# Performance work log

Hardware: AMD Instinct MI355X
Metric: run time of the kernel (lower is better)

Reference implementation:

```python
import jax, jax.numpy as jnp
import numpy as np


def _bs_matrix(n):
    # Kronecker product of n copies of the 2x2 beam-splitter unitary.
    bs = (1.0 / np.sqrt(2.0)) * np.array([[1 + 0j, 0 + 1j], [0 + 1j, 1 + 0j]], dtype=np.complex128)
    M = np.array([[1.0 + 0j]], dtype=np.complex128)
    for _ in range(n):
        M = np.kron(M, bs)
    return jnp.asarray(M, dtype=jnp.complex64)  # [2^n, 2^n]


def _phase_shifts(phi0, phi1, n):
    # Equivalent to phase_shifts_to_tensor_product_space_v2:
    # phi[i] = sum_q (phi1[q] if bit_{n-1-q}(i) else phi0[q]); returns exp(i*phi).
    N = 2 ** n
    bits = (jnp.arange(N)[:, None] >> (n - 1 - jnp.arange(n))[None, :]) & 1  # [N, n]
    bits = bits.astype(phi0.dtype)
    phi = jnp.sum(bits * phi1 + (1.0 - bits) * phi0, axis=-1)  # [N]
    return jax.lax.complex(jnp.cos(phi), jnp.sin(phi))


def setup_inputs() -> dict:
    n = 12
    N = 2 ** n
    B = 2048
    key = jax.random.key(0)
    kx, ka, kb, kt, kp = jax.random.split(key, 5)
    TWO_PI = 2.0 * np.pi
    return {
        "x": jax.random.normal(kx, (B, 2, N), dtype=jnp.float32),
        "alphas": jax.random.uniform(ka, (n,), dtype=jnp.float32, minval=0.0, maxval=TWO_PI),
        "betas": jax.random.uniform(kb, (n,), dtype=jnp.float32, minval=0.0, maxval=TWO_PI),
        "thetas": jax.random.uniform(kt, (n,), dtype=jnp.float32, minval=0.0, maxval=TWO_PI),
        "phis": jax.random.uniform(kp, (n,), dtype=jnp.float32, minval=0.0, maxval=TWO_PI),
    }


def reference(x, alphas, betas, thetas, phis):
    n = alphas.shape[0]
    bs = _bs_matrix(n)  # [N, N] complex
    input_shifts = _phase_shifts(alphas, betas, n)                       # [N]
    theta_shifts = _phase_shifts(thetas, jnp.zeros_like(thetas), n)      # [N]
    phi_shifts = _phase_shifts(phis, jnp.zeros_like(phis), n)            # [N]

    z = jax.lax.complex(x[:, 0, :], x[:, 1, :])  # [B, N]
    out = (input_shifts * z) @ bs
    out = (theta_shifts * out) @ bs
    out = phi_shifts * out
    return jnp.stack([jnp.real(out), jnp.imag(out)], axis=1)  # [B, 2, N]
```

## Files before the change

### kernel.cpp

```cpp
#include <hip/hip_runtime.h>
#include <math.h>

#define NQ 12
#define NN 4096

typedef float f2 __attribute__((ext_vector_type(2)));

__device__ __forceinline__ float2 cmulh(float2 a, float2 b) {
    return make_float2(a.x * b.x - a.y * b.y, a.x * b.y + a.y * b.x);
}

__device__ __forceinline__ void cmac_pk(f2& acc, f2 m, f2 b) {
    asm("v_pk_fma_f32 %0, %1, %2, %0 op_sel:[0,0,0] op_sel_hi:[0,1,1]\n\t"
        "v_pk_fma_f32 %0, %1, %2, %0 op_sel:[1,1,0] op_sel_hi:[1,0,1] neg_lo:[1,0,0]"
        : "+v"(acc) : "s"(m), "v"(b));
}
__device__ __forceinline__ void cmul_pk(f2& r, f2 m, f2 b) {
    asm("v_pk_mul_f32 %0, %1, %2 op_sel:[0,0] op_sel_hi:[0,1]\n\t"
        "v_pk_fma_f32 %0, %1, %2, %0 op_sel:[1,1,0] op_sel_hi:[1,0,1] neg_lo:[1,0,0]"
        : "=&v"(r) : "s"(m), "v"(b));
}

template<int D>
__device__ __forceinline__ void stagepk8(f2 (&v)[8], f2 m00, f2 m01, f2 m10, f2 m11) {
    #pragma unroll
    for (int s = 0; s < 8; ++s) {
        if (s & D) continue;
        f2 va = v[s], vb = v[s | D];
        f2 r0, r1;
        cmul_pk(r0, m00, va); cmac_pk(r0, m01, vb);
        cmul_pk(r1, m10, va); cmac_pk(r1, m11, vb);
        v[s] = r0; v[s | D] = r1;
    }
}

__global__ void setup_mats(const float* __restrict__ alphas,
                           const float* __restrict__ betas,
                           const float* __restrict__ thetas,
                           const float* __restrict__ phis,
                           float2* __restrict__ Mg) {
    int t = threadIdx.x;
    if (t < NQ) {
        int p = t, q = NQ - 1 - p;
        float sa, ca, sb, cb, st, ct, sf, cf;
        sincosf(alphas[q], &sa, &ca);
        sincosf(betas[q],  &sb, &cb);
        sincosf(thetas[q], &st, &ct);
        sincosf(phis[q],   &sf, &cf);
        float2 A  = make_float2(ca, sa);
        float2 Bb = make_float2(cb, sb);
        float2 F  = make_float2(cf, sf);
        float2 Tm  = make_float2(0.5f * (ct - 1.0f), 0.5f * st);
        float2 Tp  = make_float2(0.5f * (ct + 1.0f), 0.5f * st);
        float2 iTp = make_float2(-Tp.y, Tp.x);
        Mg[p * 4 + 0] = cmulh(cmulh(F, Tm), A);
        Mg[p * 4 + 1] = cmulh(cmulh(F, iTp), Bb);
        Mg[p * 4 + 2] = cmulh(iTp, A);
        Mg[p * 4 + 3] = cmulh(make_float2(-Tm.x, -Tm.y), Bb);
    }
}

__global__ __launch_bounds__(512, 8) void sq_layer(const float* __restrict__ x,
                                                   const float2* __restrict__ Mgf,
                                                   float* __restrict__ out) {
    __shared__ f2 lds[4608];
    const int T = threadIdx.x;
    const f2* Mg = (const f2*)Mgf;
    const size_t row0 = (size_t)blockIdx.x * 2;

    const float* px = x + row0 * (2 * NN) + (T << 3);
    float4 ra = *reinterpret_cast<const float4*>(px);
    float4 rb = *reinterpret_cast<const float4*>(px + 4);
    float4 ia = *reinterpret_cast<const float4*>(px + NN);
    float4 ib = *reinterpret_cast<const float4*>(px + NN + 4);

    #pragma unroll
    for (int r = 0; r < 2; ++r) {
        f2 v[8];
        v[0] = f2{ra.x, ia.x}; v[1] = f2{ra.y, ia.y};
        v[2] = f2{ra.z, ia.z}; v[3] = f2{ra.w, ia.w};
        v[4] = f2{rb.x, ib.x}; v[5] = f2{rb.y, ib.y};
        v[6] = f2{rb.z, ib.z}; v[7] = f2{rb.w, ib.w};

        if (r == 0) {
            const float* pn = px + 2 * NN;
            ra = *reinterpret_cast<const float4*>(pn);
            rb = *reinterpret_cast<const float4*>(pn + 4);
            ia = *reinterpret_cast<const float4*>(pn + NN);
            ib = *reinterpret_cast<const float4*>(pn + NN + 4);
        }

        stagepk8<1>(v, Mg[0],  Mg[1],  Mg[2],  Mg[3]);
        stagepk8<2>(v, Mg[4],  Mg[5],  Mg[6],  Mg[7]);
        stagepk8<4>(v, Mg[8],  Mg[9],  Mg[10], Mg[11]);

        {
            f2* wp = lds + 9 * T;
            #pragma unroll
            for (int s = 0; s < 8; ++s) wp[s] = v[s];
        }
        {
            const f2* rp = lds + 72 * (T >> 3) + (T & 7);
            #pragma unroll
            for (int s = 0; s < 8; ++s) v[s] = rp[9 * s];
        }

        stagepk8<1>(v, Mg[12], Mg[13], Mg[14], Mg[15]);
        stagepk8<2>(v, Mg[16], Mg[17], Mg[18], Mg[19]);
        stagepk8<4>(v, Mg[20], Mg[21], Mg[22], Mg[23]);

        {
            f2* wp = lds + 72 * (T >> 3) + (T & 7);
            #pragma unroll
            for (int s = 0; s < 8; ++s) wp[9 * s] = v[s];
        }
        {
            const f2* rp = lds + 576 * (T >> 6) + (T & 63) + ((T & 63) >> 3);
            #pragma unroll
            for (int s = 0; s < 8; ++s) v[s] = rp[72 * s];
        }

        stagepk8<1>(v, Mg[24], Mg[25], Mg[26], Mg[27]);
        stagepk8<2>(v, Mg[28], Mg[29], Mg[30], Mg[31]);
        stagepk8<4>(v, Mg[32], Mg[33], Mg[34], Mg[35]);

        {
            f2* wp = lds + 576 * (T >> 6) + (T & 63) + ((T & 63) >> 3);
            #pragma unroll
            for (int s = 0; s < 8; ++s) wp[72 * s] = v[s];
        }
        __syncthreads();
        {
            const f2* rp = lds + T + (T >> 3);
            #pragma unroll
            for (int s = 0; s < 8; ++s) v[s] = rp[576 * s];
        }
        if (r == 0) __syncthreads();

        stagepk8<1>(v, Mg[36], Mg[37], Mg[38], Mg[39]);
        stagepk8<2>(v, Mg[40], Mg[41], Mg[42], Mg[43]);
        stagepk8<4>(v, Mg[44], Mg[45], Mg[46], Mg[47]);

        {
            float* po = out + (row0 + r) * (2 * NN);
            #pragma unroll
            for (int s = 0; s < 8; ++s) {
                int i = (s << 9) | T;
                __builtin_nontemporal_store(v[s].x, po + i);
                __builtin_nontemporal_store(v[s].y, po + NN + i);
            }
        }
    }
}

extern "C" void kernel_launch(void* const* d_in, const int* in_sizes, int n_in,
                              void* d_out, int out_size, void* d_ws, size_t ws_size,
                              hipStream_t stream) {
    const float* x      = (const float*)d_in[0];
    const float* alphas = (const float*)d_in[1];
    const float* betas  = (const float*)d_in[2];
    const float* thetas = (const float*)d_in[3];
    const float* phis   = (const float*)d_in[4];
    float* out = (float*)d_out;
    float2* Mg = (float2*)d_ws;

    const int B = in_sizes[0] / (2 * NN);

    hipLaunchKernelGGL(setup_mats, dim3(1), dim3(64), 0, stream,
                       alphas, betas, thetas, phis, Mg);
    hipLaunchKernelGGL(sq_layer, dim3(B / 2), dim3(512), 0, stream,
                       x, (const float2*)Mg, out);
}
```

Measured before the change: 31.53 us.

## Fuse per-qubit matrix setup into main kernel via shared memory

Drops the separate setup kernel launch: each block now computes the 12 per-qubit 2x2 gate matrices itself with sincos in 12 threads, stores them in shared memory, and synchronises before use. Both rows' input loads are issued up front so their latency overlaps the setup. The inline asm operands switch from scalar to vector registers because the matrices now come from LDS. This removes one launch and its dependency gap, but every block repeats the trig work, adds a barrier, and holds more registers for the early loads.

```diff
diff --git a/kernel.cpp b/kernel.cpp
--- a/kernel.cpp
+++ b/kernel.cpp
@@ -13,12 +13,12 @@
 __device__ __forceinline__ void cmac_pk(f2& acc, f2 m, f2 b) {
     asm("v_pk_fma_f32 %0, %1, %2, %0 op_sel:[0,0,0] op_sel_hi:[0,1,1]\n\t"
         "v_pk_fma_f32 %0, %1, %2, %0 op_sel:[1,1,0] op_sel_hi:[1,0,1] neg_lo:[1,0,0]"
-        : "+v"(acc) : "s"(m), "v"(b));
+        : "+v"(acc) : "v"(m), "v"(b));
 }
 __device__ __forceinline__ void cmul_pk(f2& r, f2 m, f2 b) {
     asm("v_pk_mul_f32 %0, %1, %2 op_sel:[0,0] op_sel_hi:[0,1]\n\t"
         "v_pk_fma_f32 %0, %1, %2, %0 op_sel:[1,1,0] op_sel_hi:[1,0,1] neg_lo:[1,0,0]"
-        : "=&v"(r) : "s"(m), "v"(b));
+        : "=&v"(r) : "v"(m), "v"(b));
 }
 
 template<int D>
@@ -34,14 +34,29 @@
     }
 }
 
-__global__ void setup_mats(const float* __restrict__ alphas,
-                           const float* __restrict__ betas,
-                           const float* __restrict__ thetas,
-                           const float* __restrict__ phis,
-                           float2* __restrict__ Mg) {
-    int t = threadIdx.x;
-    if (t < NQ) {
-        int p = t, q = NQ - 1 - p;
+__global__ __launch_bounds__(512, 8) void sq_layer(const float* __restrict__ x,
+                                                   float* __restrict__ out,
+                                                   const float* __restrict__ alphas,
+                                                   const float* __restrict__ betas,
+                                                   const float* __restrict__ thetas,
+                                                   const float* __restrict__ phis) {
+    __shared__ f2 lds[4608];
+    __shared__ f2 Msh[48];
+    const int T = threadIdx.x;
+    const size_t row0 = (size_t)blockIdx.x * 2;
+
+    const float* px = x + row0 * (2 * NN) + (T << 3);
+    float4 ra0 = *reinterpret_cast<const float4*>(px);
+    float4 rb0 = *reinterpret_cast<const float4*>(px + 4);
+    float4 ia0 = *reinterpret_cast<const float4*>(px + NN);
+    float4 ib0 = *reinterpret_cast<const float4*>(px + NN + 4);
+    float4 ra1 = *reinterpret_cast<const float4*>(px + 2 * NN);
+    float4 rb1 = *reinterpret_cast<const float4*>(px + 2 * NN + 4);
+    float4 ia1 = *reinterpret_cast<const float4*>(px + 3 * NN);
+    float4 ib1 = *reinterpret_cast<const float4*>(px + 3 * NN + 4);
+
+    if (T < NQ) {
+        int p = T, q = NQ - 1 - p;
         float sa, ca, sb, cb, st, ct, sf, cf;
         sincosf(alphas[q], &sa, &ca);
         sincosf(betas[q],  &sb, &cb);
@@ -53,46 +68,32 @@
         float2 Tm  = make_float2(0.5f * (ct - 1.0f), 0.5f * st);
         float2 Tp  = make_float2(0.5f * (ct + 1.0f), 0.5f * st);
         float2 iTp = make_float2(-Tp.y, Tp.x);
-        Mg[p * 4 + 0] = cmulh(cmulh(F, Tm), A);
-        Mg[p * 4 + 1] = cmulh(cmulh(F, iTp), Bb);
-        Mg[p * 4 + 2] = cmulh(iTp, A);
-        Mg[p * 4 + 3] = cmulh(make_float2(-Tm.x, -Tm.y), Bb);
+        float2 m00 = cmulh(cmulh(F, Tm), A);
+        float2 m01 = cmulh(cmulh(F, iTp), Bb);
+        float2 m10 = cmulh(iTp, A);
+        float2 m11 = cmulh(make_float2(-Tm.x, -Tm.y), Bb);
+        Msh[p * 4 + 0] = f2{m00.x, m00.y};
+        Msh[p * 4 + 1] = f2{m01.x, m01.y};
+        Msh[p * 4 + 2] = f2{m10.x, m10.y};
+        Msh[p * 4 + 3] = f2{m11.x, m11.y};
     }
-}
-
-__global__ __launch_bounds__(512, 8) void sq_layer(const float* __restrict__ x,
-                                                   const float2* __restrict__ Mgf,
-                                                   float* __restrict__ out) {
-    __shared__ f2 lds[4608];
-    const int T = threadIdx.x;
-    const f2* Mg = (const f2*)Mgf;
-    const size_t row0 = (size_t)blockIdx.x * 2;
-
-    const float* px = x + row0 * (2 * NN) + (T << 3);
-    float4 ra = *reinterpret_cast<const float4*>(px);
-    float4 rb = *reinterpret_cast<const float4*>(px + 4);
-    float4 ia = *reinterpret_cast<const float4*>(px + NN);
-    float4 ib = *reinterpret_cast<const float4*>(px + NN + 4);
+    __syncthreads();
 
     #pragma unroll
     for (int r = 0; r < 2; ++r) {
         f2 v[8];
+        float4 ra = (r == 0) ? ra0 : ra1;
+        float4 rb = (r == 0) ? rb0 : rb1;
+        float4 ia = (r == 0) ? ia0 : ia1;
+        float4 ib = (r == 0) ? ib0 : ib1;
         v[0] = f2{ra.x, ia.x}; v[1] = f2{ra.y, ia.y};
         v[2] = f2{ra.z, ia.z}; v[3] = f2{ra.w, ia.w};
         v[4] = f2{rb.x, ib.x}; v[5] = f2{rb.y, ib.y};
         v[6] = f2{rb.z, ib.z}; v[7] = f2{rb.w, ib.w};
 
-        if (r == 0) {
-            const float* pn = px + 2 * NN;
-            ra = *reinterpret_cast<const float4*>(pn);
-            rb = *reinterpret_cast<const float4*>(pn + 4);
-            ia = *reinterpret_cast<const float4*>(pn + NN);
-            ib = *reinterpret_cast<const float4*>(pn + NN + 4);
-        }
-
-        stagepk8<1>(v, Mg[0],  Mg[1],  Mg[2],  Mg[3]);
-        stagepk8<2>(v, Mg[4],  Mg[5],  Mg[6],  Mg[7]);
-        stagepk8<4>(v, Mg[8],  Mg[9],  Mg[10], Mg[11]);
+        stagepk8<1>(v, Msh[0],  Msh[1],  Msh[2],  Msh[3]);
+        stagepk8<2>(v, Msh[4],  Msh[5],  Msh[6],  Msh[7]);
+        stagepk8<4>(v, Msh[8],  Msh[9],  Msh[10], Msh[11]);
 
         {
             f2* wp = lds + 9 * T;
@@ -105,9 +106,9 @@
             for (int s = 0; s < 8; ++s) v[s] = rp[9 * s];
         }
 
-        stagepk8<1>(v, Mg[12], Mg[13], Mg[14], Mg[15]);
-        stagepk8<2>(v, Mg[16], Mg[17], Mg[18], Mg[19]);
-        stagepk8<4>(v, Mg[20], Mg[21], Mg[22], Mg[23]);
+        stagepk8<1>(v, Msh[12], Msh[13], Msh[14], Msh[15]);
+        stagepk8<2>(v, Msh[16], Msh[17], Msh[18], Msh[19]);
+        stagepk8<4>(v, Msh[20], Msh[21], Msh[22], Msh[23]);
 
         {
             f2* wp = lds + 72 * (T >> 3) + (T & 7);
@@ -120,9 +121,9 @@
             for (int s = 0; s < 8; ++s) v[s] = rp[72 * s];
         }
 
-        stagepk8<1>(v, Mg[24], Mg[25], Mg[26], Mg[27]);
-        stagepk8<2>(v, Mg[28], Mg[29], Mg[30], Mg[31]);
-        stagepk8<4>(v, Mg[32], Mg[33], Mg[34], Mg[35]);
+        stagepk8<1>(v, Msh[24], Msh[25], Msh[26], Msh[27]);
+        stagepk8<2>(v, Msh[28], Msh[29], Msh[30], Msh[31]);
+        stagepk8<4>(v, Msh[32], Msh[33], Msh[34], Msh[35]);
 
         {
             f2* wp = lds + 576 * (T >> 6) + (T & 63) + ((T & 63) >> 3);
@@ -137,9 +138,9 @@
         }
         if (r == 0) __syncthreads();
 
-        stagepk8<1>(v, Mg[36], Mg[37], Mg[38], Mg[39]);
-        stagepk8<2>(v, Mg[40], Mg[41], Mg[42], Mg[43]);
-        stagepk8<4>(v, Mg[44], Mg[45], Mg[46], Mg[47]);
+        stagepk8<1>(v, Msh[36], Msh[37], Msh[38], Msh[39]);
+        stagepk8<2>(v, Msh[40], Msh[41], Msh[42], Msh[43]);
+        stagepk8<4>(v, Msh[44], Msh[45], Msh[46], Msh[47]);
 
         {
             float* po = out + (row0 + r) * (2 * NN);
@@ -162,12 +163,9 @@
     const float* thetas = (const float*)d_in[3];
     const float* phis   = (const float*)d_in[4];
     float* out = (float*)d_out;
-    float2* Mg = (float2*)d_ws;
 
     const int B = in_sizes[0] / (2 * NN);
 
-    hipLaunchKernelGGL(setup_mats, dim3(1), dim3(64), 0, stream,
-                       alphas, betas, thetas, phis, Mg);
     hipLaunchKernelGGL(sq_layer, dim3(B / 2), dim3(512), 0, stream,
-                       x, (const float2*)Mg, out);
+                       x, out, alphas, betas, thetas, phis);
 }
```

After: 33.11 us. 5.0% more time.
